# Kernel tuning notes

Measured on AMD Instinct MI355X. Metric: run time of the kernel, lower is better.

The kernel has to match this reference:

```python
import jax, jax.numpy as jnp
import numpy as np

LN_EPS = 1e-5

def setup_inputs() -> dict:
    key = jax.random.key(0)
    ks = jax.random.split(key, 4)
    B, T, D = 8, 2048, 1024
    x = jax.random.normal(ks[0], (B, T, D), dtype=jnp.float32)
    Wz = jax.random.normal(ks[1], (D, D), dtype=jnp.float32) * (1.0 / np.sqrt(D))
    bz = jnp.zeros((D,), dtype=jnp.float32)
    Wh = jax.random.normal(ks[2], (D, D), dtype=jnp.float32) * (1.0 / np.sqrt(D))
    bh = jnp.zeros((D,), dtype=jnp.float32)
    swish_beta = jnp.float32(1.0)
    ln_gamma = jnp.ones((D,), dtype=jnp.float32)
    ln_beta = jnp.zeros((D,), dtype=jnp.float32)
    return {"x": x, "Wz": Wz, "bz": bz, "Wh": Wh, "bh": bh,
            "swish_beta": swish_beta, "ln_gamma": ln_gamma, "ln_beta": ln_beta}

def _min_gru(x, Wz, bz, Wh, bh):
    # x: [B,T,D]. minGRU: h_t = (1-z_t)*h_{t-1} + z_t*h_tilde_t, h_0 = 0.
    z = jax.nn.sigmoid(jnp.einsum('btd,de->bte', x, Wz) + bz)   # [B,T,D]
    h_tilde = jnp.einsum('btd,de->bte', x, Wh) + bh             # [B,T,D]
    a = 1.0 - z
    b = z * h_tilde
    # parallel associative scan over time for h_t = a_t*h_{t-1} + b_t
    def combine(c1, c2):
        a1, b1 = c1
        a2, b2 = c2
        return a1 * a2, a2 * b1 + b2
    _, h = jax.lax.associative_scan(combine, (a, b), axis=1)
    return h  # [B,T,D]

def reference(x, Wz, bz, Wh, bh, swish_beta, ln_gamma, ln_beta):
    h = _min_gru(x, Wz, bz, Wh, bh)
    # Swish with learnable beta: silu(beta*x) = (beta*x)*sigmoid(beta*x)
    s = swish_beta * h
    y = s * jax.nn.sigmoid(s)
    # LayerNorm over last dim (channels_last)
    mu = jnp.mean(y, axis=-1, keepdims=True)
    var = jnp.mean(jnp.square(y - mu), axis=-1, keepdims=True)
    out = (y - mu) * jax.lax.rsqrt(var + LN_EPS) * ln_gamma + ln_beta
    return out
```

## Files before the change

kernel.cpp:

```cpp
#include <hip/hip_runtime.h>

#define GLOBAL_AS __attribute__((address_space(1)))
#define LDS_AS __attribute__((address_space(3)))

typedef unsigned short u16;
typedef unsigned int u32;
typedef __bf16 bf16x8 __attribute__((ext_vector_type(8)));
typedef float f32x4 __attribute__((ext_vector_type(4)));

static constexpr int BB = 8;
static constexpr int TT = 2048;
static constexpr int DD = 1024;
static constexpr int MM = BB * TT;
static constexpr int KK = DD;
static constexpr int NC = 64;
static constexpr int CL = TT / NC;
static constexpr int NCH = BB * NC;

__device__ __forceinline__ u16 f2bf(float f) {
  union { float f; u32 u; } c; c.f = f;
  u32 u = c.u;
  u32 r = (u + 0x7fffu + ((u >> 16) & 1u)) >> 16;
  return (u16)r;
}

__global__ void cvt_x_kernel(const float* __restrict__ x, u16* __restrict__ xb) {
  int i = (blockIdx.x * blockDim.x + threadIdx.x) * 8;
  const float4* p = reinterpret_cast<const float4*>(x + i);
  float4 v0 = p[0], v1 = p[1];
  u16 r0 = f2bf(v0.x), r1 = f2bf(v0.y), r2 = f2bf(v0.z), r3 = f2bf(v0.w);
  u16 r4 = f2bf(v1.x), r5 = f2bf(v1.y), r6 = f2bf(v1.z), r7 = f2bf(v1.w);
  uint4 o;
  o.x = (u32)r0 | ((u32)r1 << 16);
  o.y = (u32)r2 | ((u32)r3 << 16);
  o.z = (u32)r4 | ((u32)r5 << 16);
  o.w = (u32)r6 | ((u32)r7 << 16);
  *reinterpret_cast<uint4*>(xb + i) = o;
}

__global__ void cvt_w_kernel(const float* __restrict__ Wz, const float* __restrict__ Wh,
                             u16* __restrict__ WT) {
  __shared__ float tile[32][33];
  int w = blockIdx.z;
  const float* W = w ? Wh : Wz;
  u16* O = WT + (size_t)w * DD * KK;
  int k0 = blockIdx.y * 32;
  int n0 = blockIdx.x * 32;
  int tx = threadIdx.x, ty = threadIdx.y;
  for (int i = 0; i < 32; i += 8)
    tile[ty + i][tx] = W[(size_t)(k0 + ty + i) * DD + n0 + tx];
  __syncthreads();
  for (int i = 0; i < 32; i += 8)
    O[(size_t)(n0 + ty + i) * KK + k0 + tx] = f2bf(tile[tx][ty + i]);
}

__global__ __launch_bounds__(256) void gemm_dual_kernel(
    const u16* __restrict__ xb,
    const u16* __restrict__ WT,
    const float* __restrict__ bz, const float* __restrict__ bh,
    float* __restrict__ a_out, float* __restrict__ bb_out,
    float* __restrict__ Asum, float* __restrict__ Bsum) {
  __shared__ __align__(16) u16 As[128 * 32];
  __shared__ __align__(16) u16 Bzs[64 * 32];
  __shared__ __align__(16) u16 Bhs[64 * 32];

  int bid = blockIdx.x;
  int nt = bid & 15;
  int mt = bid >> 4;
  int m0 = mt * 128, n0 = nt * 64;

  int tid = threadIdx.x;
  int lane = tid & 63;
  int wave = tid >> 6;

  int drow = tid >> 2;
  int dk = (tid & 3) * 8;
  const u16* Ag0 = xb + (size_t)(m0 + drow) * KK + dk;
  const u16* Ag1 = Ag0 + (size_t)64 * KK;
  const u16* Bzg = WT + (size_t)(n0 + drow) * KK + dk;
  const u16* Bhg = Bzg + (size_t)DD * KK;

  u16* As0W = As + wave * 512;
  u16* As1W = As + 2048 + wave * 512;
  u16* BzsW = Bzs + wave * 512;
  u16* BhsW = Bhs + wave * 512;

  f32x4 accz[2][4];
  f32x4 acch[2][4];
  for (int i = 0; i < 2; i++)
    for (int j = 0; j < 4; j++) {
      accz[i][j] = (f32x4){0.f, 0.f, 0.f, 0.f};
      acch[i][j] = (f32x4){0.f, 0.f, 0.f, 0.f};
    }

  int RM = wave * 32;
  int fr = lane & 15;
  int fk = (lane >> 4) * 8;

  for (int k0i = 0; k0i < KK; k0i += 32) {
    __builtin_amdgcn_global_load_lds((const GLOBAL_AS void*)(Ag0 + k0i), (LDS_AS void*)As0W, 16, 0, 0);
    __builtin_amdgcn_global_load_lds((const GLOBAL_AS void*)(Ag1 + k0i), (LDS_AS void*)As1W, 16, 0, 0);
    __builtin_amdgcn_global_load_lds((const GLOBAL_AS void*)(Bzg + k0i), (LDS_AS void*)BzsW, 16, 0, 0);
    __builtin_amdgcn_global_load_lds((const GLOBAL_AS void*)(Bhg + k0i), (LDS_AS void*)BhsW, 16, 0, 0);
    __syncthreads();

    bf16x8 af[2], bzf[4], bhf[4];
    for (int i = 0; i < 2; i++)
      af[i] = *reinterpret_cast<const bf16x8*>(As + (RM + i * 16 + fr) * 32 + fk);
    for (int j = 0; j < 4; j++) {
      bzf[j] = *reinterpret_cast<const bf16x8*>(Bzs + (j * 16 + fr) * 32 + fk);
      bhf[j] = *reinterpret_cast<const bf16x8*>(Bhs + (j * 16 + fr) * 32 + fk);
    }
    for (int i = 0; i < 2; i++)
      for (int j = 0; j < 4; j++) {
        accz[i][j] = __builtin_amdgcn_mfma_f32_16x16x32_bf16(af[i], bzf[j], accz[i][j], 0, 0, 0);
        acch[i][j] = __builtin_amdgcn_mfma_f32_16x16x32_bf16(af[i], bhf[j], acch[i][j], 0, 0, 0);
      }
    __syncthreads();
  }

  int quad = lane >> 4;
  int cg = mt * 4 + wave;
  for (int j = 0; j < 4; j++) {
    int n = n0 + j * 16 + fr;
    float bzv = bz[n], bhv = bh[n];
    float Ai[2], Bi[2];
    for (int i = 0; i < 2; i++) {
      float Aloc = 1.f, Bloc = 0.f;
      int mbase = m0 + RM + i * 16 + quad * 4;
      for (int r = 0; r < 4; r++) {
        float zp = accz[i][j][r] + bzv;
        float hp = acch[i][j][r] + bhv;
        float zs = 1.0f / (1.0f + __expf(-zp));
        float av = 1.0f - zs;
        float bv = zs * hp;
        size_t idx = (size_t)(mbase + r) * DD + n;
        a_out[idx] = av;
        bb_out[idx] = bv;
        Bloc = av * Bloc + bv;
        Aloc = av * Aloc;
      }
      {
        float Ao = __shfl_xor(Aloc, 16, 64);
        float Bo = __shfl_xor(Bloc, 16, 64);
        float Bc = (quad & 1) ? (Aloc * Bo + Bloc) : (Ao * Bloc + Bo);
        float Ac = Aloc * Ao;
        float Ao2 = __shfl_xor(Ac, 32, 64);
        float Bo2 = __shfl_xor(Bc, 32, 64);
        Bi[i] = (quad & 2) ? (Ac * Bo2 + Bc) : (Ao2 * Bc + Bo2);
        Ai[i] = Ac * Ao2;
      }
    }
    float Ack = Ai[1] * Ai[0];
    float Bck = Ai[1] * Bi[0] + Bi[1];
    if (quad == 0) {
      Asum[(size_t)cg * DD + n] = Ack;
      Bsum[(size_t)cg * DD + n] = Bck;
    }
  }
}

__global__ void chunk_scan_kernel(const float* __restrict__ Asum, const float* __restrict__ Bsum,
                                  float* __restrict__ hin) {
  int tid = blockIdx.x * blockDim.x + threadIdx.x;
  int d = tid & (DD - 1);
  int b = tid >> 10;
  float h = 0.f;
#pragma unroll
  for (int c = 0; c < NC; c++) {
    int i = (b * NC + c) * DD + d;
    hin[i] = h;
    h = Asum[i] * h + Bsum[i];
  }
}

__global__ __launch_bounds__(256) void apply_ln_kernel(
    const float* __restrict__ a, const float* __restrict__ bb, const float* __restrict__ hin,
    const float* __restrict__ sbeta, const float* __restrict__ gamma,
    const float* __restrict__ lbeta, float* __restrict__ out) {
  __shared__ float ps[2][4];
  __shared__ float pq[2][4];
  int ch = blockIdx.x;
  int wv = threadIdx.x >> 6;
  int lane = threadIdx.x & 63;
  int d = wv * 256 + lane * 4;
  int b = ch >> 6, c = ch & (NC - 1);
  float sb = sbeta[0];

  float4 g4 = *reinterpret_cast<const float4*>(gamma + d);
  float4 be4 = *reinterpret_cast<const float4*>(lbeta + d);
  float4 h4 = *reinterpret_cast<const float4*>(hin + (size_t)ch * DD + d);

  size_t base = ((size_t)b * TT + (size_t)c * CL) * DD + d;

  float4 aR[3], bR[3];
#pragma unroll
  for (int p = 0; p < 3; p++) {
    aR[p] = *reinterpret_cast<const float4*>(a + base + (size_t)p * DD);
    bR[p] = *reinterpret_cast<const float4*>(bb + base + (size_t)p * DD);
  }

#pragma unroll
  for (int t = 0; t < CL; t++) {
    const int slot = t % 3;
    const int pslot = t & 1;
    float4 av = aR[slot], bv = bR[slot];
    h4.x = av.x * h4.x + bv.x;
    h4.y = av.y * h4.y + bv.y;
    h4.z = av.z * h4.z + bv.z;
    h4.w = av.w * h4.w + bv.w;
    if (t + 3 < CL) {
      aR[slot] = *reinterpret_cast<const float4*>(a + base + (size_t)(t + 3) * DD);
      bR[slot] = *reinterpret_cast<const float4*>(bb + base + (size_t)(t + 3) * DD);
    }
    float sx = sb * h4.x, sy = sb * h4.y, sz = sb * h4.z, sw = sb * h4.w;
    float4 y;
    y.x = sx / (1.0f + __expf(-sx));
    y.y = sy / (1.0f + __expf(-sy));
    y.z = sz / (1.0f + __expf(-sz));
    y.w = sw / (1.0f + __expf(-sw));
    float sum = y.x + y.y + y.z + y.w;
    float sq = y.x * y.x + y.y * y.y + y.z * y.z + y.w * y.w;
#pragma unroll
    for (int o = 32; o > 0; o >>= 1) {
      sum += __shfl_xor(sum, o, 64);
      sq += __shfl_xor(sq, o, 64);
    }
    if (lane == 0) { ps[pslot][wv] = sum; pq[pslot][wv] = sq; }
    __syncthreads();
    float tot = ps[pslot][0] + ps[pslot][1] + ps[pslot][2] + ps[pslot][3];
    float totq = pq[pslot][0] + pq[pslot][1] + pq[pslot][2] + pq[pslot][3];
    float mu = tot * (1.0f / DD);
    float var = totq * (1.0f / DD) - mu * mu;
    float inv = rsqrtf(fmaxf(var, 0.f) + 1e-5f);
    float4 o4;
    o4.x = (y.x - mu) * inv * g4.x + be4.x;
    o4.y = (y.y - mu) * inv * g4.y + be4.y;
    o4.z = (y.z - mu) * inv * g4.z + be4.z;
    o4.w = (y.w - mu) * inv * g4.w + be4.w;
    *reinterpret_cast<float4*>(out + base + (size_t)t * DD) = o4;
  }
}

extern "C" void kernel_launch(void* const* d_in, const int* in_sizes, int n_in,
                              void* d_out, int out_size, void* d_ws, size_t ws_size,
                              hipStream_t stream) {
  const float* x     = (const float*)d_in[0];
  const float* Wz    = (const float*)d_in[1];
  const float* bz    = (const float*)d_in[2];
  const float* Wh    = (const float*)d_in[3];
  const float* bh    = (const float*)d_in[4];
  const float* sbeta = (const float*)d_in[5];
  const float* gamma = (const float*)d_in[6];
  const float* lbeta = (const float*)d_in[7];
  float* out = (float*)d_out;

  char* ws = (char*)d_ws;
  u16* xb     = (u16*)ws;
  u16* WT     = (u16*)(ws + 33554432);
  float* bb   = (float*)(ws + 37748736);
  float* Asum = (float*)(ws + 104857600);
  float* Bsum = (float*)(ws + 106954752);
  float* hin  = (float*)(ws + 109051904);
  const size_t NEED_BASE = 111149056ull;
  const size_t NEED_FULL = NEED_BASE + 67108864ull;
  float* a_ptr = (ws_size >= NEED_FULL) ? (float*)(ws + NEED_BASE) : out;

  cvt_x_kernel<<<8192, 256, 0, stream>>>(x, xb);
  dim3 tw(32, 8), gw(32, 32, 2);
  cvt_w_kernel<<<gw, tw, 0, stream>>>(Wz, Wh, WT);
  gemm_dual_kernel<<<2048, 256, 0, stream>>>(xb, WT, bz, bh, a_ptr, bb, Asum, Bsum);
  chunk_scan_kernel<<<32, 256, 0, stream>>>(Asum, Bsum, hin);
  apply_ln_kernel<<<NCH, 256, 0, stream>>>(a_ptr, bb, hin, sbeta, gamma, lbeta, out);
}
```

Baseline: 284.7 us.

## Enlarge dual GEMM tiles to 128x128 with K=64, XOR-swizzled LDS and grid swizzle

Result: faster. 256.6 us (-9.9%).

```diff
diff --git a/kernel.cpp b/kernel.cpp
--- a/kernel.cpp
+++ b/kernel.cpp
@@ -54,80 +54,90 @@
     O[(size_t)(n0 + ty + i) * KK + k0 + tx] = f2bf(tile[tx][ty + i]);
 }
 
-__global__ __launch_bounds__(256) void gemm_dual_kernel(
+__global__ __launch_bounds__(256, 2) void gemm_dual_kernel(
     const u16* __restrict__ xb,
     const u16* __restrict__ WT,
     const float* __restrict__ bz, const float* __restrict__ bh,
     float* __restrict__ a_out, float* __restrict__ bb_out,
     float* __restrict__ Asum, float* __restrict__ Bsum) {
-  __shared__ __align__(16) u16 As[128 * 32];
-  __shared__ __align__(16) u16 Bzs[64 * 32];
-  __shared__ __align__(16) u16 Bhs[64 * 32];
+  __shared__ __align__(16) u16 As[128 * 64];
+  __shared__ __align__(16) u16 Bzs[128 * 64];
+  __shared__ __align__(16) u16 Bhs[128 * 64];
 
   int bid = blockIdx.x;
-  int nt = bid & 15;
-  int mt = bid >> 4;
-  int m0 = mt * 128, n0 = nt * 64;
+  int swz = ((bid & 7) << 7) | (bid >> 3);
+  int mt = swz >> 3;
+  int nt = swz & 7;
+  int m0 = mt * 128, n0 = nt * 128;
 
   int tid = threadIdx.x;
   int lane = tid & 63;
   int wave = tid >> 6;
-
-  int drow = tid >> 2;
-  int dk = (tid & 3) * 8;
-  const u16* Ag0 = xb + (size_t)(m0 + drow) * KK + dk;
-  const u16* Ag1 = Ag0 + (size_t)64 * KK;
-  const u16* Bzg = WT + (size_t)(n0 + drow) * KK + dk;
+  int wr = wave >> 1;
+  int wc = wave & 1;
+
+  int r0 = tid >> 3;
+  int cswz = ((tid & 7) ^ ((tid >> 3) & 7)) << 3;
+  const u16* Ag  = xb + (size_t)(m0 + r0) * KK + cswz;
+  const u16* Bzg = WT + (size_t)(n0 + r0) * KK + cswz;
   const u16* Bhg = Bzg + (size_t)DD * KK;
 
-  u16* As0W = As + wave * 512;
-  u16* As1W = As + 2048 + wave * 512;
+  u16* AsW  = As  + wave * 512;
   u16* BzsW = Bzs + wave * 512;
   u16* BhsW = Bhs + wave * 512;
 
-  f32x4 accz[2][4];
-  f32x4 acch[2][4];
-  for (int i = 0; i < 2; i++)
+  f32x4 accz[4][4];
+  f32x4 acch[4][4];
+  for (int i = 0; i < 4; i++)
     for (int j = 0; j < 4; j++) {
       accz[i][j] = (f32x4){0.f, 0.f, 0.f, 0.f};
       acch[i][j] = (f32x4){0.f, 0.f, 0.f, 0.f};
     }
 
-  int RM = wave * 32;
   int fr = lane & 15;
   int fk = (lane >> 4) * 8;
-
-  for (int k0i = 0; k0i < KK; k0i += 32) {
-    __builtin_amdgcn_global_load_lds((const GLOBAL_AS void*)(Ag0 + k0i), (LDS_AS void*)As0W, 16, 0, 0);
-    __builtin_amdgcn_global_load_lds((const GLOBAL_AS void*)(Ag1 + k0i), (LDS_AS void*)As1W, 16, 0, 0);
-    __builtin_amdgcn_global_load_lds((const GLOBAL_AS void*)(Bzg + k0i), (LDS_AS void*)BzsW, 16, 0, 0);
-    __builtin_amdgcn_global_load_lds((const GLOBAL_AS void*)(Bhg + k0i), (LDS_AS void*)BhsW, 16, 0, 0);
+  const int swx = (fr & 7) << 3;
+
+  for (int k0i = 0; k0i < KK; k0i += 64) {
+#pragma unroll
+    for (int q = 0; q < 4; q++) {
+      __builtin_amdgcn_global_load_lds((const GLOBAL_AS void*)(Ag  + k0i + (size_t)(q * 32) * KK),
+                                       (LDS_AS void*)(AsW + q * 2048), 16, 0, 0);
+      __builtin_amdgcn_global_load_lds((const GLOBAL_AS void*)(Bzg + k0i + (size_t)(q * 32) * KK),
+                                       (LDS_AS void*)(BzsW + q * 2048), 16, 0, 0);
+      __builtin_amdgcn_global_load_lds((const GLOBAL_AS void*)(Bhg + k0i + (size_t)(q * 32) * KK),
+                                       (LDS_AS void*)(BhsW + q * 2048), 16, 0, 0);
+    }
     __syncthreads();
 
-    bf16x8 af[2], bzf[4], bhf[4];
-    for (int i = 0; i < 2; i++)
-      af[i] = *reinterpret_cast<const bf16x8*>(As + (RM + i * 16 + fr) * 32 + fk);
-    for (int j = 0; j < 4; j++) {
-      bzf[j] = *reinterpret_cast<const bf16x8*>(Bzs + (j * 16 + fr) * 32 + fk);
-      bhf[j] = *reinterpret_cast<const bf16x8*>(Bhs + (j * 16 + fr) * 32 + fk);
-    }
-    for (int i = 0; i < 2; i++)
+#pragma unroll
+    for (int kk = 0; kk < 64; kk += 32) {
+      bf16x8 af[4], bzf[4], bhf[4];
+      for (int i = 0; i < 4; i++)
+        af[i] = *reinterpret_cast<const bf16x8*>(
+            As + (wr * 64 + i * 16 + fr) * 64 + ((kk + fk) ^ swx));
       for (int j = 0; j < 4; j++) {
-        accz[i][j] = __builtin_amdgcn_mfma_f32_16x16x32_bf16(af[i], bzf[j], accz[i][j], 0, 0, 0);
-        acch[i][j] = __builtin_amdgcn_mfma_f32_16x16x32_bf16(af[i], bhf[j], acch[i][j], 0, 0, 0);
+        int br = wc * 64 + j * 16 + fr;
+        bzf[j] = *reinterpret_cast<const bf16x8*>(Bzs + br * 64 + ((kk + fk) ^ swx));
+        bhf[j] = *reinterpret_cast<const bf16x8*>(Bhs + br * 64 + ((kk + fk) ^ swx));
       }
+      for (int i = 0; i < 4; i++)
+        for (int j = 0; j < 4; j++) {
+          accz[i][j] = __builtin_amdgcn_mfma_f32_16x16x32_bf16(af[i], bzf[j], accz[i][j], 0, 0, 0);
+          acch[i][j] = __builtin_amdgcn_mfma_f32_16x16x32_bf16(af[i], bhf[j], acch[i][j], 0, 0, 0);
+        }
+    }
     __syncthreads();
   }
 
   int quad = lane >> 4;
-  int cg = mt * 4 + wave;
   for (int j = 0; j < 4; j++) {
-    int n = n0 + j * 16 + fr;
+    int n = n0 + wc * 64 + j * 16 + fr;
     float bzv = bz[n], bhv = bh[n];
-    float Ai[2], Bi[2];
-    for (int i = 0; i < 2; i++) {
+    float Ai[4], Bi[4];
+    for (int i = 0; i < 4; i++) {
       float Aloc = 1.f, Bloc = 0.f;
-      int mbase = m0 + RM + i * 16 + quad * 4;
+      int mbase = m0 + wr * 64 + i * 16 + quad * 4;
       for (int r = 0; r < 4; r++) {
         float zp = accz[i][j][r] + bzv;
         float hp = acch[i][j][r] + bhv;
@@ -140,22 +150,24 @@
         Bloc = av * Bloc + bv;
         Aloc = av * Aloc;
       }
-      {
-        float Ao = __shfl_xor(Aloc, 16, 64);
-        float Bo = __shfl_xor(Bloc, 16, 64);
-        float Bc = (quad & 1) ? (Aloc * Bo + Bloc) : (Ao * Bloc + Bo);
-        float Ac = Aloc * Ao;
-        float Ao2 = __shfl_xor(Ac, 32, 64);
-        float Bo2 = __shfl_xor(Bc, 32, 64);
-        Bi[i] = (quad & 2) ? (Ac * Bo2 + Bc) : (Ao2 * Bc + Bo2);
-        Ai[i] = Ac * Ao2;
+      float Ao = __shfl_xor(Aloc, 16, 64);
+      float Bo = __shfl_xor(Bloc, 16, 64);
+      float Bc = (quad & 1) ? (Aloc * Bo + Bloc) : (Ao * Bloc + Bo);
+      float Ac = Aloc * Ao;
+      float Ao2 = __shfl_xor(Ac, 32, 64);
+      float Bo2 = __shfl_xor(Bc, 32, 64);
+      Bi[i] = (quad & 2) ? (Ac * Bo2 + Bc) : (Ao2 * Bc + Bo2);
+      Ai[i] = Ac * Ao2;
+    }
+#pragma unroll
+    for (int ic = 0; ic < 2; ic++) {
+      float Ack = Ai[2 * ic + 1] * Ai[2 * ic];
+      float Bck = Ai[2 * ic + 1] * Bi[2 * ic] + Bi[2 * ic + 1];
+      if (quad == 0) {
+        int cg = mt * 4 + wr * 2 + ic;
+        Asum[(size_t)cg * DD + n] = Ack;
+        Bsum[(size_t)cg * DD + n] = Bck;
       }
-    }
-    float Ack = Ai[1] * Ai[0];
-    float Bck = Ai[1] * Bi[0] + Bi[1];
-    if (quad == 0) {
-      Asum[(size_t)cg * DD + n] = Ack;
-      Bsum[(size_t)cg * DD + n] = Bck;
     }
   }
 }
@@ -269,7 +281,7 @@
   cvt_x_kernel<<<8192, 256, 0, stream>>>(x, xb);
   dim3 tw(32, 8), gw(32, 32, 2);
   cvt_w_kernel<<<gw, tw, 0, stream>>>(Wz, Wh, WT);
-  gemm_dual_kernel<<<2048, 256, 0, stream>>>(xb, WT, bz, bh, a_ptr, bb, Asum, Bsum);
+  gemm_dual_kernel<<<1024, 256, 0, stream>>>(xb, WT, bz, bh, a_ptr, bb, Asum, Bsum);
   chunk_scan_kernel<<<32, 256, 0, stream>>>(Asum, Bsum, hin);
   apply_ln_kernel<<<NCH, 256, 0, stream>>>(a_ptr, bb, hin, sbeta, gamma, lbeta, out);
 }
```
